# Optimization experiments

Measured on AMD Instinct MI355X. Metric: run time of the kernel, lower is better.

## Reference

```python
import jax, jax.numpy as jnp
import numpy as np

B, S, HID = 2, 2048, 2048
NH, NKV, D = 16, 8, 128
QR, KR, VR = 6, 2, 2
WIN = 1024
CAP = 50.0
EPS = 1e-6
SCALE = D ** -0.5


def setup_inputs() -> dict:
    key = jax.random.key(0)
    ks = jax.random.split(key, 12)
    w = 0.02  # weight init scale for numerical sanity
    pos = jnp.arange(S, dtype=jnp.float32)[:, None]
    inv_freq = 1.0 / (10000.0 ** (jnp.arange(0, D, 2, dtype=jnp.float32) / D))  # [D/2]
    ang = pos * inv_freq[None, :]
    return {
        "hidden_states": jax.random.normal(ks[0], (B, S, HID), jnp.float32),
        "cos": jnp.cos(ang),
        "sin": jnp.sin(ang),
        "W_A_q": jax.random.normal(ks[1], (HID, NH * QR), jnp.float32) * w,
        "W_A_k": jax.random.normal(ks[2], (HID, NKV * KR), jnp.float32) * w,
        "W_A_v": jax.random.normal(ks[3], (HID, NKV * VR), jnp.float32) * w,
        "W_B_q": jax.random.normal(ks[4], (HID, QR * D), jnp.float32) * w,
        "W_B_k": jax.random.normal(ks[5], (HID, KR * D), jnp.float32) * w,
        "W_B_v": jax.random.normal(ks[6], (HID, VR * D), jnp.float32) * w,
        "o_proj_w": jax.random.normal(ks[7], (NH * D, HID), jnp.float32) * w,
        "qnorm_w": jnp.zeros((D,), jnp.float32),  # Gemma RMSNorm: scale = 1 + w
        "knorm_w": jnp.zeros((D,), jnp.float32),
        "k_cache_A": jnp.zeros((B, S, NKV, KR), jnp.float32),
        "k_cache_B": jnp.zeros((B, S, KR, D), jnp.float32),
        "v_cache_A": jnp.zeros((B, S, NKV, VR), jnp.float32),
        "v_cache_B": jnp.zeros((B, S, VR, D), jnp.float32),
        "kv_write_indices": jnp.arange(S, dtype=jnp.int32),
    }


def _rmsnorm(x, w):
    var = jnp.mean(x * x, axis=-1, keepdims=True)
    return x * jax.lax.rsqrt(var + EPS) * (1.0 + w)


def _rope(x, cos, sin):
    # x: [B,S,R,D]; first half = real, second half = imag (torch chunk layout)
    x1, x2 = x[..., : D // 2], x[..., D // 2 :]
    c = cos[None, :, None, :]
    s = sin[None, :, None, :]
    return jnp.concatenate([x1 * c - x2 * s, x1 * s + x2 * c], axis=-1)


def reference(hidden_states, cos, sin, W_A_q, W_A_k, W_A_v, W_B_q, W_B_k, W_B_v,
              o_proj_w, qnorm_w, knorm_w, k_cache_A, k_cache_B, v_cache_A,
              v_cache_B, kv_write_indices):
    hs = hidden_states
    A_q = (hs @ W_A_q).reshape(B, S, NH, QR)
    A_k = (hs @ W_A_k).reshape(B, S, NKV, KR)
    A_v = (hs @ W_A_v).reshape(B, S, NKV, VR)
    B_q = (hs @ W_B_q).reshape(B, S, QR, D)
    B_k = (hs @ W_B_k).reshape(B, S, KR, D)
    B_v = (hs @ W_B_v).reshape(B, S, VR, D)
    # qk-norm on B factors, then RoPE on B factors
    B_q = _rope(_rmsnorm(B_q, qnorm_w), cos, sin)
    B_k = _rope(_rmsnorm(B_k, knorm_w), cos, sin)
    # KV cache write (prefill: ctx_len = kv_write_indices[-1]+1 = S, static)
    k_cache_A = k_cache_A.at[:, kv_write_indices].set(A_k)
    k_cache_B = k_cache_B.at[:, kv_write_indices].set(B_k)
    v_cache_A = v_cache_A.at[:, kv_write_indices].set(A_v)
    v_cache_B = v_cache_B.at[:, kv_write_indices].set(B_v)
    ctx = S
    # materialize Q/K/V from rank-R factors
    Q = jnp.einsum('bshr,bsrd->bhsd', A_q, B_q) / QR          # [B,NH,S,D]
    Q = Q * SCALE
    K = jnp.einsum('bskr,bsrd->bskd', k_cache_A[:, :ctx], k_cache_B[:, :ctx]) / KR
    V = jnp.einsum('bskr,bsrd->bskd', v_cache_A[:, :ctx], v_cache_B[:, :ctx]) / VR
    K = jnp.repeat(K, NH // NKV, axis=2).transpose(0, 2, 1, 3)  # [B,NH,ctx,D]
    V = jnp.repeat(V, NH // NKV, axis=2).transpose(0, 2, 1, 3)
    scores = jnp.einsum('bhqd,bhkd->bhqk', Q, K)
    scores = jnp.tanh(scores / CAP) * CAP
    # causal + sliding window mask
    i = jnp.arange(S)[:, None]
    j = jnp.arange(ctx)[None, :]
    win = min(WIN, ctx)
    allowed = (j <= i) & (j > i - win)
    min_val = jnp.finfo(scores.dtype).min
    scores = jnp.where(allowed[None, None], scores, min_val)
    attn = jax.nn.softmax(scores.astype(jnp.float32), axis=-1).astype(Q.dtype)
    out = jnp.einsum('bhqk,bhkd->bhqd', attn, V)
    out = out.transpose(0, 2, 1, 3).reshape(B, S, NH * D)
    return out @ o_proj_w
```

## Files before the change

kernel.cpp:

```cpp
#include <hip/hip_runtime.h>
#include <math.h>

#define B_    2
#define S_    2048
#define HID_  2048
#define NH_   16
#define NKV_  8
#define D_    128
#define QR_   6
#define KR_   2
#define VR_   2
#define WIN_  1024
#define CAP_  50.0f
#define EPS_  1e-6f
#define SCALE_ 0.08838834764831845f

#define OFF_AQ 0
#define OFF_AK 96
#define OFF_AV 112
#define OFF_BQ 128
#define OFF_BK 896
#define OFF_BV 1152
#define NPACK  1408

using short8 = __attribute__((ext_vector_type(8))) short;
using f32x4  = __attribute__((ext_vector_type(4))) float;
using u16x4  = __attribute__((ext_vector_type(4))) unsigned short;

__device__ __forceinline__ unsigned short f2bf(float f) {
    union { float f; unsigned u; } v; v.f = f;
    unsigned r = v.u + 0x7FFFu + ((v.u >> 16) & 1u);
    return (unsigned short)(r >> 16);
}

__device__ __forceinline__ void gload16(const unsigned short* g, unsigned short* l) {
    __builtin_amdgcn_global_load_lds(
        (const __attribute__((address_space(1))) unsigned int*)g,
        (__attribute__((address_space(3))) unsigned int*)l,
        16, 0, 0);
}

__global__ __launch_bounds__(256) void cvt_f32_bf16(const float* __restrict__ src,
                                                    unsigned short* __restrict__ dst,
                                                    int n4) {
    int i = blockIdx.x * 256 + threadIdx.x;
    if (i < n4) {
        float4 v = ((const float4*)src)[i];
        u16x4 o;
        o[0] = f2bf(v.x); o[1] = f2bf(v.y); o[2] = f2bf(v.z); o[3] = f2bf(v.w);
        ((u16x4*)dst)[i] = o;
    }
}

__global__ __launch_bounds__(256) void transpose_pack(const float* __restrict__ src,
                                                      int K, int N,
                                                      unsigned short* __restrict__ dst,
                                                      int rowOff, int dstStride) {
    __shared__ float tile[32][33];
    const int k0 = blockIdx.y * 32, n0 = blockIdx.x * 32;
    const int tx = threadIdx.x & 31, ty = threadIdx.x >> 5;
#pragma unroll
    for (int i = ty; i < 32; i += 8) {
        const int k = k0 + i, n = n0 + tx;
        tile[i][tx] = (n < N) ? src[(size_t)k * N + n] : 0.f;
    }
    __syncthreads();
#pragma unroll
    for (int i = ty; i < 32; i += 8) {
        const int n = n0 + i, k = k0 + tx;
        if (n < N) dst[(size_t)(rowOff + n) * dstStride + k] = f2bf(tile[tx][i]);
    }
}

__global__ __launch_bounds__(256) void gemm_bf16(const unsigned short* __restrict__ A,
                                                 const unsigned short* __restrict__ Bt,
                                                 float* __restrict__ C,
                                                 int M, int N, int K) {
    __shared__ unsigned short As[4096];
    __shared__ unsigned short Bs[4096];

    const int t    = threadIdx.x;
    const int lane = t & 63, wid = t >> 6;
    const int wr = wid >> 1, wc = wid & 1;
    const int row0 = blockIdx.y * 128, col0 = blockIdx.x * 128;

    const int r0 = t >> 2, g0 = t & 3;
    const int r1 = r0 + 64;
    const unsigned short* aS0 = A  + (size_t)(row0 + r0) * K + g0 * 8;
    const unsigned short* aS1 = A  + (size_t)(row0 + r1) * K + g0 * 8;
    const unsigned short* bS0 = Bt + (size_t)(col0 + r0) * K + g0 * 8;
    const unsigned short* bS1 = Bt + (size_t)(col0 + r1) * K + g0 * 8;
    unsigned short* aD0 = As + wid * 512;
    unsigned short* aD1 = As + 2048 + wid * 512;
    unsigned short* bD0 = Bs + wid * 512;
    unsigned short* bD1 = Bs + 2048 + wid * 512;

    f32x4 acc[4][4];
#pragma unroll
    for (int m = 0; m < 4; ++m)
#pragma unroll
        for (int n = 0; n < 4; ++n) { acc[m][n][0]=0.f; acc[m][n][1]=0.f; acc[m][n][2]=0.f; acc[m][n][3]=0.f; }

    const int l15 = lane & 15, kg = lane >> 4;
    int aoff[4], boff[4];
#pragma unroll
    for (int m = 0; m < 4; ++m) {
        aoff[m] = (wr * 64 + m * 16 + l15) * 32 + kg * 8;
        boff[m] = (wc * 64 + m * 16 + l15) * 32 + kg * 8;
    }

    for (int k0 = 0; k0 < K; k0 += 32) {
        __syncthreads();
        gload16(aS0 + k0, aD0);
        gload16(aS1 + k0, aD1);
        gload16(bS0 + k0, bD0);
        gload16(bS1 + k0, bD1);
        __syncthreads();
        short8 a[4], b[4];
#pragma unroll
        for (int m = 0; m < 4; ++m) a[m] = *(const short8*)(As + aoff[m]);
#pragma unroll
        for (int n = 0; n < 4; ++n) b[n] = *(const short8*)(Bs + boff[n]);
#pragma unroll
        for (int m = 0; m < 4; ++m)
#pragma unroll
            for (int n = 0; n < 4; ++n)
                acc[m][n] = __builtin_amdgcn_mfma_f32_16x16x32_bf16(a[m], b[n], acc[m][n], 0, 0, 0);
    }

#pragma unroll
    for (int m = 0; m < 4; ++m) {
#pragma unroll
        for (int n = 0; n < 4; ++n) {
            const int cc = col0 + wc * 64 + n * 16 + l15;
#pragma unroll
            for (int q = 0; q < 4; ++q) {
                const int rr = row0 + wr * 64 + m * 16 + kg * 4 + q;
                C[(size_t)rr * N + cc] = acc[m][n][q];
            }
        }
    }
}

__global__ __launch_bounds__(64) void norm_rope(float* __restrict__ Cp,
                                                int colOff, int R,
                                                const float* __restrict__ w,
                                                const float* __restrict__ cosT,
                                                const float* __restrict__ sinT) {
    const int blk = blockIdx.x;
    const int bs = blk / R, r = blk % R;
    const int s = bs % S_;
    const int l = threadIdx.x;
    float* v = Cp + (size_t)bs * NPACK + colOff + r * D_;
    float x1 = v[l];
    float x2 = v[l + 64];
    float ss = x1 * x1 + x2 * x2;
#pragma unroll
    for (int off = 32; off; off >>= 1) ss += __shfl_xor(ss, off);
    const float inv = 1.0f / sqrtf(ss * (1.0f / 128.0f) + EPS_);
    x1 *= inv * (1.0f + w[l]);
    x2 *= inv * (1.0f + w[l + 64]);
    const float c  = cosT[s * 64 + l];
    const float sn = sinT[s * 64 + l];
    v[l]      = x1 * c - x2 * sn;
    v[l + 64] = x1 * sn + x2 * c;
}

__global__ __launch_bounds__(256) void scatter_kernel(const float* __restrict__ Cp,
                                                      const int* __restrict__ idx,
                                                      float* __restrict__ eKA,
                                                      float* __restrict__ eKB,
                                                      float* __restrict__ eVA,
                                                      float* __restrict__ eVB) {
    const int bs = blockIdx.x;
    const int b  = bs / S_;
    const int s  = bs % S_;
    const int di = idx[s];
    const size_t dst = (size_t)b * S_ + di;
    const int t = threadIdx.x;
    const float* rowp = Cp + (size_t)bs * NPACK;
    if (t < 16) { eKA[dst * 16 + t] = rowp[OFF_AK + t]; eVA[dst * 16 + t] = rowp[OFF_AV + t]; }
    eKB[dst * 256 + t] = rowp[OFF_BK + t];
    eVB[dst * 256 + t] = rowp[OFF_BV + t];
}

__global__ __launch_bounds__(256) void assemble_kernel(const float* __restrict__ Cp,
                                                       const float* __restrict__ eKA,
                                                       const float* __restrict__ eKB,
                                                       const float* __restrict__ eVA,
                                                       const float* __restrict__ eVB,
                                                       unsigned short* __restrict__ Qo,
                                                       unsigned short* __restrict__ Ko,
                                                       unsigned short* __restrict__ Vo) {
    __shared__ float aq[96];
    __shared__ float bq[768];
    __shared__ float ka[16];
    __shared__ float kb[256];
    __shared__ float va[16];
    __shared__ float vb[256];

    const int bs = blockIdx.x;
    const int b  = bs / S_;
    const int s  = bs % S_;
    const int t  = threadIdx.x;
    const float* rowp = Cp + (size_t)bs * NPACK;

    if (t < 96) aq[t] = rowp[OFF_AQ + t];
    for (int i = t; i < 768; i += 256) bq[i] = rowp[OFF_BQ + i];
    if (t < 16) { ka[t] = eKA[(size_t)bs * 16 + t]; va[t] = eVA[(size_t)bs * 16 + t]; }
    kb[t] = eKB[(size_t)bs * 256 + t];
    vb[t] = eVB[(size_t)bs * 256 + t];
    __syncthreads();

    const float qf = SCALE_ / (float)QR_;
#pragma unroll
    for (int i = 0; i < 8; ++i) {
        const int o = t + 256 * i;
        const int h = o >> 7, d = o & 127;
        float acc = 0.f;
#pragma unroll
        for (int r = 0; r < QR_; ++r) acc = fmaf(aq[h * QR_ + r], bq[r * D_ + d], acc);
        Qo[(((size_t)b * NH_ + h) * S_ + s) * D_ + d] = f2bf(acc * qf);
    }
#pragma unroll
    for (int i = 0; i < 4; ++i) {
        const int o = t + 256 * i;
        const int g = o >> 7, d = o & 127;
        const float kk = 0.5f * (ka[g * 2 + 0] * kb[d] + ka[g * 2 + 1] * kb[D_ + d]);
        const float vv = 0.5f * (va[g * 2 + 0] * vb[d] + va[g * 2 + 1] * vb[D_ + d]);
        Ko[(((size_t)b * NKV_ + g) * S_ + s) * D_ + d] = f2bf(kk);
        Vo[(((size_t)b * NKV_ + g) * S_ + s) * D_ + d] = f2bf(vv);
    }
}

__global__ __launch_bounds__(256) void transpose_v(const unsigned short* __restrict__ Vn,
                                                   unsigned short* __restrict__ Vt) {
    __shared__ unsigned short ts[64][72];
    const int s0 = blockIdx.x * 64;
    const int d0 = blockIdx.y * 64;
    const int bk = blockIdx.z;
    const unsigned short* src = Vn + (size_t)bk * S_ * D_;
    unsigned short* dst = Vt + (size_t)bk * D_ * S_;
    const int t = threadIdx.x;
#pragma unroll
    for (int u = 0; u < 2; ++u) {
        const int sl = t + 256 * u;
        const int r = sl >> 3, g = sl & 7;
        *(short8*)&ts[r][g * 8] = *(const short8*)(src + (size_t)(s0 + r) * D_ + d0 + g * 8);
    }
    __syncthreads();
#pragma unroll
    for (int u = 0; u < 2; ++u) {
        const int sl = t + 256 * u;
        const int d = sl >> 3, g = sl & 7;
        short8 v;
#pragma unroll
        for (int e = 0; e < 8; ++e) v[e] = (short)ts[g * 8 + e][d];
        *(short8*)(dst + (size_t)(d0 + d) * S_ + s0 + g * 8) = v;
    }
}

__global__ __launch_bounds__(256) void attn_mfma(const unsigned short* __restrict__ Q,
                                                 const unsigned short* __restrict__ K,
                                                 const unsigned short* __restrict__ Vt,
                                                 unsigned short* __restrict__ O) {
    __shared__ unsigned short Ks[64 * 128];
    __shared__ unsigned short Vts[128 * 64];
    __shared__ unsigned short Ps[4][16 * 64];

    const int qt = blockIdx.x, h = blockIdx.y, b = blockIdx.z;
    const int kv = h >> 1;
    const int q0 = qt * 64;
    const int t = threadIdx.x;
    const int lane = t & 63, wid = t >> 6;
    const int l15 = lane & 15, kg = lane >> 4;

    const unsigned short* Qb = Q  + (size_t)(b * NH_  + h)  * S_ * D_;
    const unsigned short* Kb = K  + (size_t)(b * NKV_ + kv) * S_ * D_;
    const unsigned short* Vb = Vt + (size_t)(b * NKV_ + kv) * (size_t)D_ * S_;

    short8 qfrag[4];
#pragma unroll
    for (int c = 0; c < 4; ++c)
        qfrag[c] = *(const short8*)(Qb + (size_t)(q0 + wid * 16 + l15) * D_ + c * 32 + kg * 8);

    int ksSlot[4], vsSlot[4];
    size_t ksSrc[4], vsSrc[4];
#pragma unroll
    for (int u = 0; u < 4; ++u) {
        const int s = t + 256 * u;
        const int key = s >> 4, gp = s & 15, g = gp ^ (key & 7);
        ksSlot[u] = s * 8;
        ksSrc[u]  = (size_t)key * D_ + g * 8;
        const int d = s >> 3, gp2 = s & 7, g2 = gp2 ^ (d & 7);
        vsSlot[u] = s * 8;
        vsSrc[u]  = (size_t)d * S_ + g2 * 8;
    }

    const int kstart  = (q0 - (WIN_ - 1) > 0) ? (q0 - (WIN_ - 1)) : 0;
    const int k_begin = kstart & ~63;
    const int nt = (q0 + 64 - k_begin) >> 6;

    short8 kreg[4], vreg[4];
#pragma unroll
    for (int u = 0; u < 4; ++u) {
        kreg[u] = *(const short8*)(Kb + (size_t)k_begin * D_ + ksSrc[u]);
        vreg[u] = *(const short8*)(Vb + (size_t)k_begin + vsSrc[u]);
    }

    float l_run[4] = {0.f, 0.f, 0.f, 0.f};
    f32x4 oacc[8];
#pragma unroll
    for (int n = 0; n < 8; ++n) { oacc[n][0] = 0.f; oacc[n][1] = 0.f; oacc[n][2] = 0.f; oacc[n][3] = 0.f; }

    unsigned short* Pw = &Ps[wid][0];
    const int gi_base = q0 + wid * 16 + kg * 4;

    for (int ti = 0; ti < nt; ++ti) {
        const int k0 = k_begin + ti * 64;
        __syncthreads();
#pragma unroll
        for (int u = 0; u < 4; ++u) {
            *(short8*)(Ks  + ksSlot[u]) = kreg[u];
            *(short8*)(Vts + vsSlot[u]) = vreg[u];
        }
        __syncthreads();
        if (ti + 1 < nt) {
            const int k1 = k0 + 64;
#pragma unroll
            for (int u = 0; u < 4; ++u) {
                kreg[u] = *(const short8*)(Kb + (size_t)k1 * D_ + ksSrc[u]);
                vreg[u] = *(const short8*)(Vb + (size_t)k1 + vsSrc[u]);
            }
        }

        f32x4 sacc[4];
#pragma unroll
        for (int n = 0; n < 4; ++n) { sacc[n][0] = 0.f; sacc[n][1] = 0.f; sacc[n][2] = 0.f; sacc[n][3] = 0.f; }
#pragma unroll
        for (int c = 0; c < 4; ++c) {
#pragma unroll
            for (int n = 0; n < 4; ++n) {
                const short8 bf = *(const short8*)(Ks + (n * 16 + l15) * 128 + (((4 * c + kg) ^ (l15 & 7)) * 8));
                sacc[n] = __builtin_amdgcn_mfma_f32_16x16x32_bf16(qfrag[c], bf, sacc[n], 0, 0, 0);
            }
        }

        float p[4][4];
#pragma unroll
        for (int q = 0; q < 4; ++q) {
            const int gi = gi_base + q;
#pragma unroll
            for (int n = 0; n < 4; ++n) {
                const float e  = __expf(sacc[n][q] * (2.0f / CAP_));
                const float r  = __builtin_amdgcn_rcpf(e + 1.0f);
                const int  gj  = k0 + n * 16 + l15;
                const bool ok  = (gj <= gi) && (gj > gi - WIN_);
                const float pv = ok ? __expf(fmaf(-2.0f * CAP_, r, CAP_)) : 0.f;
                p[n][q] = pv;
                l_run[q] += pv;
            }
        }

#pragma unroll
        for (int n = 0; n < 4; ++n)
#pragma unroll
            for (int q = 0; q < 4; ++q) {
                const int r = kg * 4 + q;
                Pw[r * 64 + (((2 * n + (l15 >> 3)) ^ (r & 7)) * 8) + (l15 & 7)] = f2bf(p[n][q]);
            }

#pragma unroll
        for (int c = 0; c < 2; ++c) {
            const short8 af = *(const short8*)(Pw + l15 * 64 + (((4 * c + kg) ^ (l15 & 7)) * 8));
#pragma unroll
            for (int n = 0; n < 8; ++n) {
                const int d = n * 16 + l15;
                const short8 bfv = *(const short8*)(Vts + d * 64 + (((4 * c + kg) ^ (d & 7)) * 8));
                oacc[n] = __builtin_amdgcn_mfma_f32_16x16x32_bf16(af, bfv, oacc[n], 0, 0, 0);
            }
        }
    }

#pragma unroll
    for (int q = 0; q < 4; ++q) {
        float ls = l_run[q];
        ls += __shfl_xor(ls, 1);
        ls += __shfl_xor(ls, 2);
        ls += __shfl_xor(ls, 4);
        ls += __shfl_xor(ls, 8);
        const float il = (ls > 0.f) ? 1.0f / ls : 0.f;
        unsigned short* orow = O + (size_t)(b * S_ + gi_base + q) * (NH_ * D_) + h * D_;
#pragma unroll
        for (int n = 0; n < 8; ++n)
            orow[n * 16 + l15] = f2bf(oacc[n][q] * il);
    }
}

extern "C" void kernel_launch(void* const* d_in, const int* in_sizes, int n_in,
                              void* d_out, int out_size, void* d_ws, size_t ws_size,
                              hipStream_t stream) {
    const float* hs   = (const float*)d_in[0];
    const float* cosT = (const float*)d_in[1];
    const float* sinT = (const float*)d_in[2];
    const float* WAq  = (const float*)d_in[3];
    const float* WAk  = (const float*)d_in[4];
    const float* WAv  = (const float*)d_in[5];
    const float* WBq  = (const float*)d_in[6];
    const float* WBk  = (const float*)d_in[7];
    const float* WBv  = (const float*)d_in[8];
    const float* Wo   = (const float*)d_in[9];
    const float* qnw  = (const float*)d_in[10];
    const float* knw  = (const float*)d_in[11];
    const float* kcA  = (const float*)d_in[12];
    const float* kcB  = (const float*)d_in[13];
    const float* vcA  = (const float*)d_in[14];
    const float* vcB  = (const float*)d_in[15];
    const int*   kidx = (const int*)d_in[16];
    float* out = (float*)d_out;

    const size_t MROW = (size_t)B_ * S_;
    char* w = (char*)d_ws;
    auto alloc = [&](size_t bytes) { char* r = w; w += (bytes + 255) & ~(size_t)255; return r; };

    unsigned short* hsbf = (unsigned short*)alloc(MROW * HID_ * 2);
    unsigned short* Wt   = (unsigned short*)alloc((size_t)NPACK * HID_ * 2);
    unsigned short* Wto  = (unsigned short*)alloc((size_t)HID_ * HID_ * 2);
    float* Cp  = (float*)alloc(MROW * NPACK * 4);
    float* eKA = (float*)alloc(MROW * 16 * 4);
    float* eKB = (float*)alloc(MROW * 256 * 4);
    float* eVA = (float*)alloc(MROW * 16 * 4);
    float* eVB = (float*)alloc(MROW * 256 * 4);
    unsigned short* Qbf = (unsigned short*)alloc((size_t)B_ * NH_  * S_ * D_ * 2);
    unsigned short* Kbf = (unsigned short*)alloc((size_t)B_ * NKV_ * S_ * D_ * 2);
    unsigned short* Vbf = (unsigned short*)alloc((size_t)B_ * NKV_ * S_ * D_ * 2);
    unsigned short* Vtb = (unsigned short*)alloc((size_t)B_ * NKV_ * S_ * D_ * 2);
    unsigned short* aObf = (unsigned short*)alloc(MROW * (NH_ * D_) * 2);

    const int M = (int)MROW;

    cvt_f32_bf16<<<(M * HID_ / 4 + 255) / 256, 256, 0, stream>>>(hs, hsbf, M * HID_ / 4);
    transpose_pack<<<dim3( 3, 64), 256, 0, stream>>>(WAq, HID_,   96, Wt, OFF_AQ, HID_);
    transpose_pack<<<dim3( 1, 64), 256, 0, stream>>>(WAk, HID_,   16, Wt, OFF_AK, HID_);
    transpose_pack<<<dim3( 1, 64), 256, 0, stream>>>(WAv, HID_,   16, Wt, OFF_AV, HID_);
    transpose_pack<<<dim3(24, 64), 256, 0, stream>>>(WBq, HID_,  768, Wt, OFF_BQ, HID_);
    transpose_pack<<<dim3( 8, 64), 256, 0, stream>>>(WBk, HID_,  256, Wt, OFF_BK, HID_);
    transpose_pack<<<dim3( 8, 64), 256, 0, stream>>>(WBv, HID_,  256, Wt, OFF_BV, HID_);
    transpose_pack<<<dim3(64, 64), 256, 0, stream>>>(Wo,  HID_, 2048, Wto, 0,     HID_);

    gemm_bf16<<<dim3(NPACK / 128, M / 128), 256, 0, stream>>>(hsbf, Wt, Cp, M, NPACK, HID_);

    norm_rope<<<M * QR_, 64, 0, stream>>>(Cp, OFF_BQ, QR_, qnw, cosT, sinT);
    norm_rope<<<M * KR_, 64, 0, stream>>>(Cp, OFF_BK, KR_, knw, cosT, sinT);

    hipMemcpyAsync(eKA, kcA, MROW * 16  * 4, hipMemcpyDeviceToDevice, stream);
    hipMemcpyAsync(eKB, kcB, MROW * 256 * 4, hipMemcpyDeviceToDevice, stream);
    hipMemcpyAsync(eVA, vcA, MROW * 16  * 4, hipMemcpyDeviceToDevice, stream);
    hipMemcpyAsync(eVB, vcB, MROW * 256 * 4, hipMemcpyDeviceToDevice, stream);
    scatter_kernel<<<M, 256, 0, stream>>>(Cp, kidx, eKA, eKB, eVA, eVB);

    assemble_kernel<<<M, 256, 0, stream>>>(Cp, eKA, eKB, eVA, eVB, Qbf, Kbf, Vbf);
    transpose_v<<<dim3(S_ / 64, D_ / 64, B_ * NKV_), 256, 0, stream>>>(Vbf, Vtb);

    attn_mfma<<<dim3(S_ / 64, NH_, B_), 256, 0, stream>>>(Qbf, Kbf, Vtb, aObf);

    gemm_bf16<<<dim3(HID_ / 128, M / 128), 256, 0, stream>>>(aObf, Wto, out, M, HID_, HID_);
}
```

Before: 395.7 us.

## Merge small launches, rework V transpose, reorder attention grid heavy-first

Merges the seven weight transposes into one launch, the two norm/rope launches into one, and the four cache memcpys into a single copy kernel, which cuts launch overhead. The V transpose now handles the whole 128-wide head dim per block, packing pairs of bf16 into 32-bit LDS words with an XOR swizzle to reduce bank conflicts. The attention grid is remapped so that heads and batch vary fastest and query tiles are issued in reverse order, so the most expensive tiles start first. The merged kernels launch some idle blocks that exit early.

```diff
diff --git a/kernel.cpp b/kernel.cpp
--- a/kernel.cpp
+++ b/kernel.cpp
@@ -52,12 +52,30 @@
     }
 }
 
-__global__ __launch_bounds__(256) void transpose_pack(const float* __restrict__ src,
-                                                      int K, int N,
-                                                      unsigned short* __restrict__ dst,
-                                                      int rowOff, int dstStride) {
+__global__ __launch_bounds__(256) void pack_weights(const float* __restrict__ s0,
+                                                    const float* __restrict__ s1,
+                                                    const float* __restrict__ s2,
+                                                    const float* __restrict__ s3,
+                                                    const float* __restrict__ s4,
+                                                    const float* __restrict__ s5,
+                                                    const float* __restrict__ s6,
+                                                    unsigned short* __restrict__ Wt,
+                                                    unsigned short* __restrict__ Wto) {
     __shared__ float tile[32][33];
-    const int k0 = blockIdx.y * 32, n0 = blockIdx.x * 32;
+    const int seg = blockIdx.z;
+    const float* src; int N, rowOff; unsigned short* dst;
+    switch (seg) {
+        case 0:  src = s0; N =   96; rowOff = OFF_AQ; dst = Wt;  break;
+        case 1:  src = s1; N =   16; rowOff = OFF_AK; dst = Wt;  break;
+        case 2:  src = s2; N =   16; rowOff = OFF_AV; dst = Wt;  break;
+        case 3:  src = s3; N =  768; rowOff = OFF_BQ; dst = Wt;  break;
+        case 4:  src = s4; N =  256; rowOff = OFF_BK; dst = Wt;  break;
+        case 5:  src = s5; N =  256; rowOff = OFF_BV; dst = Wt;  break;
+        default: src = s6; N = 2048; rowOff = 0;      dst = Wto; break;
+    }
+    const int n0 = blockIdx.x * 32;
+    if (n0 >= N) return;
+    const int k0 = blockIdx.y * 32;
     const int tx = threadIdx.x & 31, ty = threadIdx.x >> 5;
 #pragma unroll
     for (int i = ty; i < 32; i += 8) {
@@ -68,7 +86,7 @@
 #pragma unroll
     for (int i = ty; i < 32; i += 8) {
         const int n = n0 + i, k = k0 + tx;
-        if (n < N) dst[(size_t)(rowOff + n) * dstStride + k] = f2bf(tile[tx][i]);
+        if (n < N) dst[(size_t)(rowOff + n) * HID_ + k] = f2bf(tile[tx][i]);
     }
 }
 
@@ -142,12 +160,17 @@
     }
 }
 
-__global__ __launch_bounds__(64) void norm_rope(float* __restrict__ Cp,
-                                                int colOff, int R,
-                                                const float* __restrict__ w,
-                                                const float* __restrict__ cosT,
-                                                const float* __restrict__ sinT) {
+__global__ __launch_bounds__(64) void norm_rope_all(float* __restrict__ Cp,
+                                                    const float* __restrict__ qnw,
+                                                    const float* __restrict__ knw,
+                                                    const float* __restrict__ cosT,
+                                                    const float* __restrict__ sinT) {
+    const int which = blockIdx.y;
+    const int R = which ? KR_ : QR_;
     const int blk = blockIdx.x;
+    if (blk >= B_ * S_ * R) return;
+    const int colOff = which ? OFF_BK : OFF_BQ;
+    const float* w = which ? knw : qnw;
     const int bs = blk / R, r = blk % R;
     const int s = bs % S_;
     const int l = threadIdx.x;
@@ -164,6 +187,26 @@
     const float sn = sinT[s * 64 + l];
     v[l]      = x1 * c - x2 * sn;
     v[l + 64] = x1 * sn + x2 * c;
+}
+
+__global__ __launch_bounds__(256) void copy_caches(const float4* __restrict__ kA,
+                                                   const float4* __restrict__ kB,
+                                                   const float4* __restrict__ vA,
+                                                   const float4* __restrict__ vB,
+                                                   float4* __restrict__ eA,
+                                                   float4* __restrict__ eB,
+                                                   float4* __restrict__ eC,
+                                                   float4* __restrict__ eD) {
+    const int NA = B_ * S_ * 16 / 4;
+    const int NB = B_ * S_ * 256 / 4;
+    int i = blockIdx.x * 256 + threadIdx.x;
+    if (i < NA)                { eA[i] = kA[i]; return; }
+    i -= NA;
+    if (i < NB)                { eB[i] = kB[i]; return; }
+    i -= NB;
+    if (i < NA)                { eC[i] = vA[i]; return; }
+    i -= NA;
+    if (i < NB)                { eD[i] = vB[i]; }
 }
 
 __global__ __launch_bounds__(256) void scatter_kernel(const float* __restrict__ Cp,
@@ -235,28 +278,41 @@
 
 __global__ __launch_bounds__(256) void transpose_v(const unsigned short* __restrict__ Vn,
                                                    unsigned short* __restrict__ Vt) {
-    __shared__ unsigned short ts[64][72];
+    __shared__ unsigned int ts32[128][36];
     const int s0 = blockIdx.x * 64;
-    const int d0 = blockIdx.y * 64;
     const int bk = blockIdx.z;
     const unsigned short* src = Vn + (size_t)bk * S_ * D_;
     unsigned short* dst = Vt + (size_t)bk * D_ * S_;
     const int t = threadIdx.x;
+    const int dg  = t & 15;
+    const int spq = t >> 4;
+
 #pragma unroll
     for (int u = 0; u < 2; ++u) {
-        const int sl = t + 256 * u;
-        const int r = sl >> 3, g = sl & 7;
-        *(short8*)&ts[r][g * 8] = *(const short8*)(src + (size_t)(s0 + r) * D_ + d0 + g * 8);
+        const int sp = u * 16 + spq;
+        const short8 a = *(const short8*)(src + (size_t)(s0 + 2 * sp)     * D_ + dg * 8);
+        const short8 b = *(const short8*)(src + (size_t)(s0 + 2 * sp + 1) * D_ + dg * 8);
+#pragma unroll
+        for (int e = 0; e < 8; ++e) {
+            const int d = dg * 8 + e;
+            const unsigned int val = ((unsigned int)(unsigned short)a[e])
+                                   | (((unsigned int)(unsigned short)b[e]) << 16);
+            ts32[d][sp ^ (4 * (dg & 7))] = val;
+        }
     }
     __syncthreads();
 #pragma unroll
-    for (int u = 0; u < 2; ++u) {
-        const int sl = t + 256 * u;
-        const int d = sl >> 3, g = sl & 7;
-        short8 v;
-#pragma unroll
-        for (int e = 0; e < 8; ++e) v[e] = (short)ts[g * 8 + e][d];
-        *(short8*)(dst + (size_t)(d0 + d) * S_ + s0 + g * 8) = v;
+    for (int u = 0; u < 4; ++u) {
+        const int slot = t + 256 * u;
+        const int d = slot >> 3, sg = slot & 7;
+        const int cb = (sg * 4) ^ (4 * ((d >> 3) & 7));
+        const uint4 v = *(const uint4*)&ts32[d][cb];
+        short8 o;
+        o[0] = (short)(v.x & 0xffff); o[1] = (short)(v.x >> 16);
+        o[2] = (short)(v.y & 0xffff); o[3] = (short)(v.y >> 16);
+        o[4] = (short)(v.z & 0xffff); o[5] = (short)(v.z >> 16);
+        o[6] = (short)(v.w & 0xffff); o[7] = (short)(v.w >> 16);
+        *(short8*)(dst + (size_t)d * S_ + s0 + sg * 8) = o;
     }
 }
 
@@ -268,7 +324,9 @@
     __shared__ unsigned short Vts[128 * 64];
     __shared__ unsigned short Ps[4][16 * 64];
 
-    const int qt = blockIdx.x, h = blockIdx.y, b = blockIdx.z;
+    const int hb = blockIdx.x;
+    const int h = hb & 15, b = hb >> 4;
+    const int qt = 31 - (int)blockIdx.y;
     const int kv = h >> 1;
     const int q0 = qt * 64;
     const int t = threadIdx.x;
@@ -440,29 +498,25 @@
     const int M = (int)MROW;
 
     cvt_f32_bf16<<<(M * HID_ / 4 + 255) / 256, 256, 0, stream>>>(hs, hsbf, M * HID_ / 4);
-    transpose_pack<<<dim3( 3, 64), 256, 0, stream>>>(WAq, HID_,   96, Wt, OFF_AQ, HID_);
-    transpose_pack<<<dim3( 1, 64), 256, 0, stream>>>(WAk, HID_,   16, Wt, OFF_AK, HID_);
-    transpose_pack<<<dim3( 1, 64), 256, 0, stream>>>(WAv, HID_,   16, Wt, OFF_AV, HID_);
-    transpose_pack<<<dim3(24, 64), 256, 0, stream>>>(WBq, HID_,  768, Wt, OFF_BQ, HID_);
-    transpose_pack<<<dim3( 8, 64), 256, 0, stream>>>(WBk, HID_,  256, Wt, OFF_BK, HID_);
-    transpose_pack<<<dim3( 8, 64), 256, 0, stream>>>(WBv, HID_,  256, Wt, OFF_BV, HID_);
-    transpose_pack<<<dim3(64, 64), 256, 0, stream>>>(Wo,  HID_, 2048, Wto, 0,     HID_);
+    pack_weights<<<dim3(64, 64, 7), 256, 0, stream>>>(WAq, WAk, WAv, WBq, WBk, WBv, Wo, Wt, Wto);
 
     gemm_bf16<<<dim3(NPACK / 128, M / 128), 256, 0, stream>>>(hsbf, Wt, Cp, M, NPACK, HID_);
 
-    norm_rope<<<M * QR_, 64, 0, stream>>>(Cp, OFF_BQ, QR_, qnw, cosT, sinT);
-    norm_rope<<<M * KR_, 64, 0, stream>>>(Cp, OFF_BK, KR_, knw, cosT, sinT);
-
-    hipMemcpyAsync(eKA, kcA, MROW * 16  * 4, hipMemcpyDeviceToDevice, stream);
-    hipMemcpyAsync(eKB, kcB, MROW * 256 * 4, hipMemcpyDeviceToDevice, stream);
-    hipMemcpyAsync(eVA, vcA, MROW * 16  * 4, hipMemcpyDeviceToDevice, stream);
-    hipMemcpyAsync(eVB, vcB, MROW * 256 * 4, hipMemcpyDeviceToDevice, stream);
+    norm_rope_all<<<dim3(M * QR_, 2), 64, 0, stream>>>(Cp, qnw, knw, cosT, sinT);
+
+    {
+        const int NA = B_ * S_ * 16 / 4, NB = B_ * S_ * 256 / 4;
+        const int total = 2 * NA + 2 * NB;
+        copy_caches<<<(total + 255) / 256, 256, 0, stream>>>(
+            (const float4*)kcA, (const float4*)kcB, (const float4*)vcA, (const float4*)vcB,
+            (float4*)eKA, (float4*)eKB, (float4*)eVA, (float4*)eVB);
+    }
     scatter_kernel<<<M, 256, 0, stream>>>(Cp, kidx, eKA, eKB, eVA, eVB);
 
     assemble_kernel<<<M, 256, 0, stream>>>(Cp, eKA, eKB, eVA, eVB, Qbf, Kbf, Vbf);
-    transpose_v<<<dim3(S_ / 64, D_ / 64, B_ * NKV_), 256, 0, stream>>>(Vbf, Vtb);
-
-    attn_mfma<<<dim3(S_ / 64, NH_, B_), 256, 0, stream>>>(Qbf, Kbf, Vtb, aObf);
+    transpose_v<<<dim3(S_ / 64, 1, B_ * NKV_), 256, 0, stream>>>(Vbf, Vtb);
+
+    attn_mfma<<<dim3(32, 32, 1), 256, 0, stream>>>(Qbf, Kbf, Vtb, aObf);
 
     gemm_bf16<<<dim3(HID_ / 128, M / 128), 256, 0, stream>>>(aObf, Wto, out, M, HID_, HID_);
 }
```

Result: faster. 372.6 us (-5.8%).
